# Optimization experiments

Measured on AMD Instinct MI355X. Metric: run time of the kernel, lower is better.

## Reference

```python
import jax, jax.numpy as jnp
import numpy as np

C = 256      # d_model
H = 8        # nhead
DF = 1024    # dim_feedforward
LE = 2048    # ego tokens
LA = 2048    # other-agent tokens
N_MATCH = 1024


def setup_inputs() -> dict:
    key = jax.random.key(0)
    ks = jax.random.split(key, 16)
    def rn(k, shape, s=0.02):
        return jax.random.normal(k, shape, dtype=jnp.float32) * s
    inp = {}
    inp['x_ego'] = jax.random.normal(ks[0], (LE, C), dtype=jnp.float32)
    inp['x_agent'] = jax.random.normal(ks[1], (LA, C), dtype=jnp.float32)
    # query_fusion MLP(2C -> C -> C -> C), torch Linear weight is (out, in)
    inp['Wf1'] = rn(ks[2], (C, 2 * C)); inp['bf1'] = jnp.zeros((C,), jnp.float32)
    inp['Wf2'] = rn(ks[3], (C, C));     inp['bf2'] = jnp.zeros((C,), jnp.float32)
    inp['Wf3'] = rn(ks[4], (C, C));     inp['bf3'] = jnp.zeros((C,), jnp.float32)
    # nn.MultiheadAttention packed in-proj and out-proj
    inp['Wqkv'] = rn(ks[5], (3 * C, C)); inp['bqkv'] = jnp.zeros((3 * C,), jnp.float32)
    inp['Wo'] = rn(ks[6], (C, C));       inp['bo'] = jnp.zeros((C,), jnp.float32)
    # FFN
    inp['W1'] = rn(ks[7], (DF, C)); inp['b1'] = jnp.zeros((DF,), jnp.float32)
    inp['W2'] = rn(ks[8], (C, DF)); inp['b2'] = jnp.zeros((C,), jnp.float32)
    # LayerNorms
    inp['g1'] = jnp.ones((C,), jnp.float32); inp['be1'] = jnp.zeros((C,), jnp.float32)
    inp['g2'] = jnp.ones((C,), jnp.float32); inp['be2'] = jnp.zeros((C,), jnp.float32)
    # unique 1D positions: first N_MATCH agent positions overlap ego, rest don't
    inp['pos_ego'] = jnp.arange(LE, dtype=jnp.int32)
    pa = np.concatenate([np.arange(N_MATCH), np.arange(LA - N_MATCH) + 10_000_000])
    inp['pos_agent'] = jnp.asarray(pa, dtype=jnp.int32)
    inp['n_remain'] = LA - N_MATCH  # static python int
    return inp


def _ln(t, g, b):
    m = t.mean(-1, keepdims=True)
    v = t.var(-1, keepdims=True)
    return (t - m) / jnp.sqrt(v + 1e-5) * g + b


def reference(x_ego, x_agent, Wf1, bf1, Wf2, bf2, Wf3, bf3, Wqkv, bqkv, Wo, bo,
              W1, b1, W2, b2, g1, be1, g2, be2, pos_ego, pos_agent, n_remain):
    # ---- position-keyed grouping / fuse (replaces the host-side dict loop) ----
    eq = pos_agent[:, None] == pos_ego[None, :]          # [La, Le]
    matched_e = eq.any(axis=0)                           # ego token has same-pos agent token
    agent_for_ego = jnp.argmax(eq, axis=0)               # [Le] matching agent index (valid where matched)
    fused_in = jnp.concatenate([x_ego, x_agent[agent_for_ego]], axis=-1)  # [Le, 2C]
    h = jax.nn.relu(fused_in @ Wf1.T + bf1)
    h = jax.nn.relu(h @ Wf2.T + bf2)
    fused = h @ Wf3.T + bf3                              # query_fusion MLP output [Le, C]
    ego_out = jnp.where(matched_e[:, None], fused, x_ego)
    # agent tokens with no ego match, in original agent order (fixed count n_remain)
    remain_idx = jnp.nonzero(~eq.any(axis=1), size=n_remain)[0]
    q = jnp.concatenate([ego_out, x_agent[remain_idx]], axis=0)[None]  # (1, Lq, C)
    kv = jnp.concatenate([x_ego, x_agent], axis=0)[None]               # (1, Lk, C)
    # ---- MultiheadAttention (batch_first, eval: dropout off) ----
    Wq, Wk, Wv = jnp.split(Wqkv, 3, axis=0)
    bq, bk, bv = jnp.split(bqkv, 3, axis=0)
    dh = C // H
    def heads(t, W, b):
        return (t @ W.T + b).reshape(1, -1, H, dh).transpose(0, 2, 1, 3)
    qh, kh, vh = heads(q, Wq, bq), heads(kv, Wk, bk), heads(kv, Wv, bv)
    scores = jnp.einsum('bhqd,bhkd->bhqk', qh, kh) / (float(dh) ** 0.5)
    attn = jax.nn.softmax(scores, axis=-1)
    o = jnp.einsum('bhqk,bhkd->bhqd', attn, vh).transpose(0, 2, 1, 3).reshape(1, -1, C)
    o = o @ Wo.T + bo
    # ---- residual + norm1 + FFN + residual + norm2 ----
    yq = _ln(q + o, g1, be1)
    ff = jax.nn.relu(yq @ W1.T + b1) @ W2.T + b2
    return _ln(yq + ff, g2, be2)
```

## Files before the change

### kernel.cpp

```cpp
#include <hip/hip_runtime.h>


#define LE 2048
#define LA 2048
#define CDIM 256
#define HN 8
#define DH 32
#define DFF 1024
#define NREM 1024
#define LQC 3072
#define LKC 4096
#define KSPLIT 8
#define NIT (LKC / KSPLIT / 64)

typedef unsigned short u16;
typedef unsigned int u32;
typedef __attribute__((ext_vector_type(8))) short bf16x8;
typedef __attribute__((ext_vector_type(4))) float f32x4;

__device__ __forceinline__ u32 pk_bf16(float a, float b) {
    u32 ua = (__builtin_bit_cast(u32, a) + 0x8000u) >> 16;
    u32 ub = (__builtin_bit_cast(u32, b) + 0x8000u) >> 16;
    return ua | (ub << 16);
}
__device__ __forceinline__ u16 bf16_1(float a) {
    return (u16)((__builtin_bit_cast(u32, a) + 0x8000u) >> 16);
}
__device__ __forceinline__ float fast_exp2(float x) {
    return __builtin_amdgcn_exp2f(x);
}
__device__ __forceinline__ bf16x8 ld_pack8(const float* p) {
    float4 f0 = *(const float4*)p;
    float4 f1 = *(const float4*)(p + 4);
    union { u32 u[4]; bf16x8 v; } o;
    o.u[0] = pk_bf16(f0.x, f0.y); o.u[1] = pk_bf16(f0.z, f0.w);
    o.u[2] = pk_bf16(f1.x, f1.y); o.u[3] = pk_bf16(f1.z, f1.w);
    return o.v;
}

__device__ __forceinline__ void xcd_tile(int& bm, int& bn) {
    int gx = gridDim.x;
    int tot = gx * gridDim.y;
    int p = blockIdx.y * gx + blockIdx.x;
    int l = p;
    if (!(tot & 7)) { int c = p & 7, s = p >> 3; l = c * (tot >> 3) + s; }
    bm = (l / gx) * 64;
    bn = (l % gx) * 64;
}

struct WPtrs { const float* p[7]; };
__constant__ __device__ const int woff[8] = {0, 131072, 196608, 262144,
                                             458752, 524288, 786432, 1048576};

__global__ __launch_bounds__(1024) void k_prep(const int* __restrict__ pos_ego,
                                               const int* __restrict__ pos_agent,
                                               int* __restrict__ afe,
                                               int* __restrict__ matched,
                                               int* __restrict__ remain,
                                               const float* __restrict__ x_ego,
                                               const float* __restrict__ x_agent,
                                               WPtrs wp, u16* __restrict__ wb,
                                               u16* __restrict__ kv_b) {
    const int b = blockIdx.x;
    const int t = threadIdx.x;
    if (b == 0) {
        __shared__ int keyA[4096], valA[4096], keyE[4096];
        __shared__ int unm[2048];
#pragma unroll
        for (int i = 0; i < 4; ++i) { keyA[t + i * 1024] = -1; keyE[t + i * 1024] = -1; }
        __syncthreads();
// ... 63 lines not shown
#pragma unroll
        for (int i = 1; i < 7; ++i) s += (g >= woff[i]);
        const float* src = wp.p[s] + (g - woff[s]);
        float4 f0 = *(const float4*)(src);
        float4 f1 = *(const float4*)(src + 4);
        uint4 o;
        o.x = pk_bf16(f0.x, f0.y); o.y = pk_bf16(f0.z, f0.w);
        o.z = pk_bf16(f1.x, f1.y); o.w = pk_bf16(f1.z, f1.w);
        *(uint4*)(wb + g) = o;
    } else {
        int tt = (b - 129) * 1024 + t;
        int j = tt >> 5, c8 = tt & 31;
        const float* src = (j < LE) ? (x_ego + (size_t)j * CDIM)
                                    : (x_agent + (size_t)(j - LE) * CDIM);
        float4 f0 = *(const float4*)(src + c8 * 8);
        float4 f1 = *(const float4*)(src + c8 * 8 + 4);
        uint4 o;
        o.x = pk_bf16(f0.x, f0.y); o.y = pk_bf16(f0.z, f0.w);
        o.z = pk_bf16(f1.x, f1.y); o.w = pk_bf16(f1.z, f1.w);
        *(uint4*)(kv_b + (size_t)j * CDIM + c8 * 8) = o;
    }
}

template <int EPI, bool RELU>
__global__ __launch_bounds__(256) void gemm_bf16(const u16* __restrict__ A,
                                                 const u16* __restrict__ B,
                                                 const float* __restrict__ bias,
                                                 void* __restrict__ C,
                                                 int M, int N, int K) {
    const int tid = threadIdx.x;
    const int w = tid >> 6, lane = tid & 63;
    const int quad = lane >> 4, qi = lane & 15;
    const int wm = w >> 1, wn = w & 1;
    int bm, bn;
    xcd_tile(bm, bn);

    const u16* pa0 = A + (size_t)(bm + wm * 32 + qi) * K + quad * 8;
    const u16* pa1 = pa0 + (size_t)16 * K;
    const u16* pb0 = B + (size_t)(bn + wn * 32 + qi) * K + quad * 8;
    const u16* pb1 = pb0 + (size_t)16 * K;

    f32x4 acc00 = {0.f, 0.f, 0.f, 0.f}, acc01 = {0.f, 0.f, 0.f, 0.f};
    f32x4 acc10 = {0.f, 0.f, 0.f, 0.f}, acc11 = {0.f, 0.f, 0.f, 0.f};

#pragma unroll 4
    for (int k = 0; k < K; k += 32) {
        bf16x8 a0 = *(const bf16x8*)(pa0 + k);
        bf16x8 a1 = *(const bf16x8*)(pa1 + k);
        bf16x8 b0 = *(const bf16x8*)(pb0 + k);
        bf16x8 b1 = *(const bf16x8*)(pb1 + k);
        acc00 = __builtin_amdgcn_mfma_f32_16x16x32_bf16(a0, b0, acc00, 0, 0, 0);
        acc01 = __builtin_amdgcn_mfma_f32_16x16x32_bf16(a0, b1, acc01, 0, 0, 0);
        acc10 = __builtin_amdgcn_mfma_f32_16x16x32_bf16(a1, b0, acc10, 0, 0, 0);
        acc11 = __builtin_amdgcn_mfma_f32_16x16x32_bf16(a1, b1, acc11, 0, 0, 0);
    }

#pragma unroll
    for (int i = 0; i < 2; ++i) {
#pragma unroll
        for (int j = 0; j < 2; ++j) {
            f32x4 acc = (i == 0) ? (j == 0 ? acc00 : acc01) : (j == 0 ? acc10 : acc11);
            int n = bn + wn * 32 + j * 16 + qi;
            int mbase = bm + wm * 32 + i * 16 + quad * 4;
            float bs = bias[n];
            float v[4];
#pragma unroll
            for (int r = 0; r < 4; ++r) {
                float x = acc[r] + bs;
                if (RELU) x = fmaxf(x, 0.f);
                v[r] = x;
            }
            if (EPI == 0) {
                float* Cf = (float*)C;
#pragma unroll
                for (int r = 0; r < 4; ++r) Cf[(size_t)(mbase + r) * N + n] = v[r];
            } else {
                u16* Cb = (u16*)C;
#pragma unroll
                for (int r = 0; r < 4; ++r) Cb[(size_t)(mbase + r) * N + n] = bf16_1(v[r]);
            }
        }
    }
}

__global__ __launch_bounds__(256) void k_mlp1(const float* __restrict__ x_ego,
                                              const float* __restrict__ x_agent,
                                              const int* __restrict__ afe,
                                              const u16* __restrict__ Wf1_b,
                                              const float* __restrict__ bf1,
                                              u16* __restrict__ h1_b) {
    const int tid = threadIdx.x;
    const int w = tid >> 6, lane = tid & 63;
    const int quad = lane >> 4, qi = lane & 15;
    const int wm = w >> 1, wn = w & 1;
    int bm, bn;
    xcd_tile(bm, bn);

    const int r0 = bm + wm * 32 + qi, r1 = r0 + 16;
    const float* pe0 = x_ego + (size_t)r0 * CDIM + quad * 8;
    const float* pe1 = x_ego + (size_t)r1 * CDIM + quad * 8;
    const float* pg0 = x_agent + (size_t)afe[r0] * CDIM + quad * 8;
    const float* pg1 = x_agent + (size_t)afe[r1] * CDIM + quad * 8;
    const u16* pb0 = Wf1_b + (size_t)(bn + wn * 32 + qi) * 512 + quad * 8;
    const u16* pb1 = pb0 + (size_t)16 * 512;

    f32x4 acc00 = {0.f, 0.f, 0.f, 0.f}, acc01 = {0.f, 0.f, 0.f, 0.f};
    f32x4 acc10 = {0.f, 0.f, 0.f, 0.f}, acc11 = {0.f, 0.f, 0.f, 0.f};

#pragma unroll 4
    for (int k = 0; k < 256; k += 32) {
        bf16x8 a0 = ld_pack8(pe0 + k);
        bf16x8 a1 = ld_pack8(pe1 + k);
        bf16x8 b0 = *(const bf16x8*)(pb0 + k);
        bf16x8 b1 = *(const bf16x8*)(pb1 + k);
        acc00 = __builtin_amdgcn_mfma_f32_16x16x32_bf16(a0, b0, acc00, 0, 0, 0);
        acc01 = __builtin_amdgcn_mfma_f32_16x16x32_bf16(a0, b1, acc01, 0, 0, 0);
        acc10 = __builtin_amdgcn_mfma_f32_16x16x32_bf16(a1, b0, acc10, 0, 0, 0);
        acc11 = __builtin_amdgcn_mfma_f32_16x16x32_bf16(a1, b1, acc11, 0, 0, 0);
    }
#pragma unroll 4
    for (int k = 0; k < 256; k += 32) {
        bf16x8 a0 = ld_pack8(pg0 + k);
        bf16x8 a1 = ld_pack8(pg1 + k);
        bf16x8 b0 = *(const bf16x8*)(pb0 + 256 + k);
        bf16x8 b1 = *(const bf16x8*)(pb1 + 256 + k);
        acc00 = __builtin_amdgcn_mfma_f32_16x16x32_bf16(a0, b0, acc00, 0, 0, 0);
        acc01 = __builtin_amdgcn_mfma_f32_16x16x32_bf16(a0, b1, acc01, 0, 0, 0);
        acc10 = __builtin_amdgcn_mfma_f32_16x16x32_bf16(a1, b0, acc10, 0, 0, 0);
        acc11 = __builtin_amdgcn_mfma_f32_16x16x32_bf16(a1, b1, acc11, 0, 0, 0);
    }
#pragma unroll
    for (int i = 0; i < 2; ++i)
#pragma unroll
        for (int j = 0; j < 2; ++j) {
            f32x4 acc = (i == 0) ? (j == 0 ? acc00 : acc01) : (j == 0 ? acc10 : acc11);
            int n = bn + wn * 32 + j * 16 + qi;
            int mbase = bm + wm * 32 + i * 16 + quad * 4;
            float bs = bf1[n];
#pragma unroll
            for (int r = 0; r < 4; ++r) {
                float x = fmaxf(acc[r] + bs, 0.f);
                h1_b[(size_t)(mbase + r) * 256 + n] = bf16_1(x);
            }
        }
}

__global__ __launch_bounds__(256) void k_mlp3f(const u16* __restrict__ h2_b,
                                               const u16* __restrict__ Wf3_b,
                                               const float* __restrict__ bf3,
                                               const int* __restrict__ matched,
                                               const int* __restrict__ remain,
                                               const float* __restrict__ x_ego,
                                               const float* __restrict__ x_agent,
                                               float* __restrict__ qbuf,
                                               u16* __restrict__ qbuf_b) {
    const int tid = threadIdx.x;
    int bm, bn;
    xcd_tile(bm, bn);
    if (bm >= LE) {
        int row = bm + (tid >> 2);
        int col = bn + (tid & 3) * 16;
        int idx = remain[row - LE];
        idx = min(max(idx, 0), LA - 1);
        const float* src = x_agent + (size_t)idx * CDIM + col;
        float* dq = qbuf + (size_t)row * CDIM + col;
        u16* db = qbuf_b + (size_t)row * CDIM + col;
#pragma unroll
        for (int i = 0; i < 4; ++i) {
            float4 v = *(const float4*)(src + i * 4);
            *(float4*)(dq + i * 4) = v;
            *(uint2*)(db + i * 4) = make_uint2(pk_bf16(v.x, v.y), pk_bf16(v.z, v.w));
        }
        return;
    }
    const int w = tid >> 6, lane = tid & 63;
    const int quad = lane >> 4, qi = lane & 15;
    const int wm = w >> 1, wn = w & 1;
    const u16* pa0 = h2_b + (size_t)(bm + wm * 32 + qi) * 256 + quad * 8;
    const u16* pa1 = pa0 + (size_t)16 * 256;
    const u16* pb0 = Wf3_b + (size_t)(bn + wn * 32 + qi) * 256 + quad * 8;
    const u16* pb1 = pb0 + (size_t)16 * 256;
    f32x4 a00 = {0, 0, 0, 0}, a01 = {0, 0, 0, 0}, a10 = {0, 0, 0, 0}, a11 = {0, 0, 0, 0};
#pragma unroll 4
    for (int k = 0; k < 256; k += 32) {
        bf16x8 x0 = *(const bf16x8*)(pa0 + k);
        bf16x8 x1 = *(const bf16x8*)(pa1 + k);
        bf16x8 y0 = *(const bf16x8*)(pb0 + k);
        bf16x8 y1 = *(const bf16x8*)(pb1 + k);
        a00 = __builtin_amdgcn_mfma_f32_16x16x32_bf16(x0, y0, a00, 0, 0, 0);
        a01 = __builtin_amdgcn_mfma_f32_16x16x32_bf16(x0, y1, a01, 0, 0, 0);
        a10 = __builtin_amdgcn_mfma_f32_16x16x32_bf16(x1, y0, a10, 0, 0, 0);
        a11 = __builtin_amdgcn_mfma_f32_16x16x32_bf16(x1, y1, a11, 0, 0, 0);
    }
#pragma unroll
    for (int i = 0; i < 2; ++i)
#pragma unroll
        for (int jj = 0; jj < 2; ++jj) {
            f32x4 acc = (i == 0) ? (jj == 0 ? a00 : a01) : (jj == 0 ? a10 : a11);
            int n = bn + wn * 32 + jj * 16 + qi;
            int mb = bm + wm * 32 + i * 16 + quad * 4;
            float bs = bf3[n];
#pragma unroll
            for (int r = 0; r < 4; ++r) {
                int row = mb + r;
                float v = acc[r] + bs;
                if (!matched[row]) v = x_ego[(size_t)row * CDIM + n];
                qbuf[(size_t)row * CDIM + n] = v;
                qbuf_b[(size_t)row * CDIM + n] = bf16_1(v);
            }
        }
}

__global__ __launch_bounds__(256) void k_qkv(const u16* __restrict__ qbuf_b,
                                             const u16* __restrict__ kv_b,
                                             const u16* __restrict__ Wq,
                                             const u16* __restrict__ Wkv,
                                             const float* __restrict__ bqkv,
                                             u16* __restrict__ qb,
                                             u16* __restrict__ kbp,
                                             u16* __restrict__ vtb,
                                             float qscale) {
    int b;
    {
        int p = blockIdx.x;
        int c = p & 7, s = p >> 3;
        b = c * 88 + s;
    }
    const u16 *A, *B;
    const float* bias;
    int bm, bn, mode;
    if (b < 192) {
        A = qbuf_b; B = Wq; bias = bqkv;
        bm = (b >> 2) * 64; bn = (b & 3) * 64; mode = 0;
// ... 1 lines not shown
        int c = b - 192;
        A = kv_b; B = Wkv; bias = bqkv + 256;
        bm = (c >> 3) * 64; bn = (c & 7) * 64; mode = 1;
    }
    const int tid = threadIdx.x;
    const int w = tid >> 6, lane = tid & 63;
    const int quad = lane >> 4, qi = lane & 15;
    const int wm = w >> 1, wn = w & 1;
    const int K = 256;

    const u16* pa0 = A + (size_t)(bm + wm * 32 + qi) * K + quad * 8;
    const u16* pa1 = pa0 + (size_t)16 * K;
    const u16* pb0 = B + (size_t)(bn + wn * 32 + qi) * K + quad * 8;
    const u16* pb1 = pb0 + (size_t)16 * K;

    f32x4 acc00 = {0.f, 0.f, 0.f, 0.f}, acc01 = {0.f, 0.f, 0.f, 0.f};
    f32x4 acc10 = {0.f, 0.f, 0.f, 0.f}, acc11 = {0.f, 0.f, 0.f, 0.f};
#pragma unroll 4
    for (int k = 0; k < 256; k += 32) {
        bf16x8 a0 = *(const bf16x8*)(pa0 + k);
        bf16x8 a1 = *(const bf16x8*)(pa1 + k);
        bf16x8 b0 = *(const bf16x8*)(pb0 + k);
        bf16x8 b1 = *(const bf16x8*)(pb1 + k);
        acc00 = __builtin_amdgcn_mfma_f32_16x16x32_bf16(a0, b0, acc00, 0, 0, 0);
        acc01 = __builtin_amdgcn_mfma_f32_16x16x32_bf16(a0, b1, acc01, 0, 0, 0);
        acc10 = __builtin_amdgcn_mfma_f32_16x16x32_bf16(a1, b0, acc10, 0, 0, 0);
        acc11 = __builtin_amdgcn_mfma_f32_16x16x32_bf16(a1, b1, acc11, 0, 0, 0);
    }
#pragma unroll
    for (int i = 0; i < 2; ++i) {
#pragma unroll
        for (int j = 0; j < 2; ++j) {
            f32x4 acc = (i == 0) ? (j == 0 ? acc00 : acc01) : (j == 0 ? acc10 : acc11);
            int n = bn + wn * 32 + j * 16 + qi;
            int mbase = bm + wm * 32 + i * 16 + quad * 4;
            float bs = bias[n];
            float v[4];
#pragma unroll
            for (int r = 0; r < 4; ++r) v[r] = acc[r] + bs;
            if (mode == 0) {
#pragma unroll
                for (int r = 0; r < 4; ++r)
                    qb[(size_t)(mbase + r) * 256 + n] = bf16_1(v[r] * qscale);
            } else if (n < 256) {
#pragma unroll
                for (int r = 0; r < 4; ++r)
                    kbp[(size_t)(mbase + r) * 256 + n] = bf16_1(v[r]);
            } else {
                ushort4 o4;
                o4.x = bf16_1(v[0]); o4.y = bf16_1(v[1]);
// ... 50 lines not shown

    int kt = ks * (LKC / KSPLIT);
    {
        bf16x8 kr = *(const bf16x8*)(kg0 + (size_t)kt * CDIM);
        bf16x8 vr = *(const bf16x8*)(vg0 + kt);
        *(bf16x8*)&Kt[0][kdst] = kr;
        *(bf16x8*)&Vt[0][vdst] = vr;
    }
    int buf = 0;
    for (int it = 0; it < NIT; ++it, kt += 64) {
        __syncthreads();
        bf16x8 knext, vnext;
        const bool more = (it + 1 < NIT);
        if (more) {
            knext = *(const bf16x8*)(kg0 + (size_t)(kt + 64) * CDIM);
            vnext = *(const bf16x8*)(vg0 + kt + 64);
        }

        bf16x8 a0 = *(const bf16x8*)&Kt[buf][ka0];
        bf16x8 a1 = *(const bf16x8*)&Kt[buf][ka0 + 16 * 32];
        bf16x8 a2 = *(const bf16x8*)&Kt[buf][ka0 + 32 * 32];
        bf16x8 a3 = *(const bf16x8*)&Kt[buf][ka0 + 48 * 32];
        f32x4 z = {0.f, 0.f, 0.f, 0.f};
        f32x4 s0 = __builtin_amdgcn_mfma_f32_16x16x32_bf16(a0, qf, z, 0, 0, 0);
        f32x4 s1 = __builtin_amdgcn_mfma_f32_16x16x32_bf16(a1, qf, z, 0, 0, 0);
        f32x4 s2 = __builtin_amdgcn_mfma_f32_16x16x32_bf16(a2, qf, z, 0, 0, 0);
        f32x4 s3 = __builtin_amdgcn_mfma_f32_16x16x32_bf16(a3, qf, z, 0, 0, 0);

        float p0[4], p1[4], p2[4], p3[4];
#pragma unroll
        for (int r = 0; r < 4; ++r) {
            p0[r] = fast_exp2(s0[r]); p1[r] = fast_exp2(s1[r]);
            p2[r] = fast_exp2(s2[r]); p3[r] = fast_exp2(s3[r]);
            lsum += p0[r] + p1[r] + p2[r] + p3[r];
        }

        u16* pb = &plds[w][0];
#pragma unroll
        for (int t2 = 0; t2 < 4; ++t2) {
            int jg = t2 * 2 + (quad >> 1);
            int off = qi * 64 + ((jg ^ swz) << 3) + half;
            uint2 pw;
            float* pp = (t2 == 0) ? p0 : (t2 == 1) ? p1 : (t2 == 2) ? p2 : p3;
            pw.x = pk_bf16(pp[0], pp[1]);
            pw.y = pk_bf16(pp[2], pp[3]);
            *(uint2*)&pb[off] = pw;
        }
        bf16x8 pa0 = *(bf16x8*)&pb[rd0];
        bf16x8 pa1 = *(bf16x8*)&pb[rd1];

        bf16x8 v00 = *(const bf16x8*)&Vt[buf][v00o];
        bf16x8 v01 = *(const bf16x8*)&Vt[buf][v01o];
        bf16x8 v10 = *(const bf16x8*)&Vt[buf][v00o + 16 * 64];
        bf16x8 v11 = *(const bf16x8*)&Vt[buf][v01o + 16 * 64];
        O0 = __builtin_amdgcn_mfma_f32_16x16x32_bf16(pa0, v00, O0, 0, 0, 0);
        O0 = __builtin_amdgcn_mfma_f32_16x16x32_bf16(pa1, v01, O0, 0, 0, 0);
        O1 = __builtin_amdgcn_mfma_f32_16x16x32_bf16(pa0, v10, O1, 0, 0, 0);
        O1 = __builtin_amdgcn_mfma_f32_16x16x32_bf16(pa1, v11, O1, 0, 0, 0);

        if (more) {
            *(bf16x8*)&Kt[buf ^ 1][kdst] = knext;
            *(bf16x8*)&Vt[buf ^ 1][vdst] = vnext;
        }
        buf ^= 1;
    }

    lsum += __shfl_xor(lsum, 16, 64);
    lsum += __shfl_xor(lsum, 32, 64);

    int pbase = (h * KSPLIT + ks) * LQC + q0;
    if (quad == 0) Pl[pbase + qi] = lsum;
#pragma unroll
    for (int r = 0; r < 4; ++r) {
        int q = quad * 4 + r;
        u16* pa = Pacc + (size_t)(pbase + q) * 32;
        pa[qi] = __builtin_bit_cast(u16, (_Float16)O0[r]);
        pa[16 + qi] = __builtin_bit_cast(u16, (_Float16)O1[r]);
    }
}

__global__ __launch_bounds__(256) void attn_combine(const float* __restrict__ Pl,
                                                    const u16* __restrict__ Pacc,
                                                    u16* __restrict__ attn_b) {
    int t = blockIdx.x * 256 + threadIdx.x;
    int row = t >> 6;
    int h = (t >> 3) & 7;
    int d4 = t & 7;
    float L = 0.f;
    float o[4] = {};
#pragma unroll
    for (int ck = 0; ck < KSPLIT; ++ck) {
        size_t pidx = (size_t)(h * KSPLIT + ck) * LQC + row;
        L += Pl[pidx];
        ushort4 a = *(const ushort4*)(Pacc + pidx * 32 + d4 * 4);
        o[0] += (float)__builtin_bit_cast(_Float16, a.x);
        o[1] += (float)__builtin_bit_cast(_Float16, a.y);
        o[2] += (float)__builtin_bit_cast(_Float16, a.z);
        o[3] += (float)__builtin_bit_cast(_Float16, a.w);
    }
    float inv = 1.0f / L;
    ushort4 ov;
    ov.x = bf16_1(o[0] * inv); ov.y = bf16_1(o[1] * inv);
    ov.z = bf16_1(o[2] * inv); ov.w = bf16_1(o[3] * inv);
    *(ushort4*)(attn_b + (size_t)row * CDIM + h * DH + d4 * 4) = ov;
}

template <bool EMIT_BF16>
__global__ __launch_bounds__(256) void ln_kernel(const float* __restrict__ X,
                                                 const float* __restrict__ R,
                                                 const float* __restrict__ g,
                                                 const float* __restrict__ b,
                                                 float* __restrict__ out,
                                                 u16* __restrict__ out_b) {
    int lane = threadIdx.x & 63;
    int row = blockIdx.x * 4 + (threadIdx.x >> 6);
    const float* x = X + (size_t)row * CDIM;
    const float* r = R + (size_t)row * CDIM;
    float4 xv = *(const float4*)(x + lane * 4);
    float4 rv = *(const float4*)(r + lane * 4);
    float v[4] = {xv.x + rv.x, xv.y + rv.y, xv.z + rv.z, xv.w + rv.w};
    float s = v[0] + v[1] + v[2] + v[3];
    float sq = v[0] * v[0] + v[1] * v[1] + v[2] * v[2] + v[3] * v[3];
#pragma unroll
    for (int off = 32; off >= 1; off >>= 1) {
        s += __shfl_xor(s, off, 64);
        sq += __shfl_xor(sq, off, 64);
    }
    float mean = s * (1.f / 256.f);
    float var = sq * (1.f / 256.f) - mean * mean;
    float rstd = rsqrtf(var + 1e-5f);
    float4 gv = *(const float4*)(g + lane * 4);
    float4 bv = *(const float4*)(b + lane * 4);
    float4 o = make_float4((v[0] - mean) * rstd * gv.x + bv.x,
                           (v[1] - mean) * rstd * gv.y + bv.y,
                           (v[2] - mean) * rstd * gv.z + bv.z,
                           (v[3] - mean) * rstd * gv.w + bv.w);
    *(float4*)(out + (size_t)row * CDIM + lane * 4) = o;
    if (EMIT_BF16) {
        uint2 ob;
        ob.x = pk_bf16(o.x, o.y);
        ob.y = pk_bf16(o.z, o.w);
        *(uint2*)(out_b + (size_t)row * CDIM + lane * 4) = ob;
    }
}

extern "C" void kernel_launch(void* const* d_in, const int* in_sizes, int n_in,
                              void* d_out, int out_size, void* d_ws, size_t ws_size,
                              hipStream_t stream) {
    const float* x_ego = (const float*)d_in[0];
    const float* x_agent = (const float*)d_in[1];
    const float* Wf1 = (const float*)d_in[2];
    const float* bf1 = (const float*)d_in[3];
    const float* Wf2 = (const float*)d_in[4];
    const float* bf2 = (const float*)d_in[5];
    const float* Wf3 = (const float*)d_in[6];
    const float* bf3 = (const float*)d_in[7];
    const float* Wqkv = (const float*)d_in[8];
    const float* bqkv = (const float*)d_in[9];
    const float* Wo = (const float*)d_in[10];
    const float* bo = (const float*)d_in[11];
    const float* W1 = (const float*)d_in[12];
    const float* b1 = (const float*)d_in[13];
    const float* W2 = (const float*)d_in[14];
    const float* b2 = (const float*)d_in[15];
    const float* g1 = (const float*)d_in[16];
    const float* be1 = (const float*)d_in[17];
    const float* g2 = (const float*)d_in[18];
    const float* be2 = (const float*)d_in[19];
    const int* pos_ego = (const int*)d_in[20];
    const int* pos_agent = (const int*)d_in[21];

    float* ws = (float*)d_ws;
    size_t o = 0;
    float* qbuf = ws + o; o += 786432;
    float* o2 = ws + o; o += 786432;
    float* yq = ws + o; o += 786432;
    float* ff2 = o2;
    float* Pl = ws + o; o += HN * KSPLIT * LQC;
    u16* Pacc = (u16*)(ws + o); o += (size_t)HN * KSPLIT * LQC * 16;
    u16* wb = (u16*)(ws + o); o += 524288;
    u16* h1_b = (u16*)(ws + o); o += 262144;
    u16* h2_b = (u16*)(ws + o); o += 262144;
    u16* qbuf_b = (u16*)(ws + o); o += 393216;
    u16* kv_b = (u16*)(ws + o); o += 524288;
    u16* qb = (u16*)(ws + o); o += 393216;
    u16* kb = (u16*)(ws + o); o += 524288;
    u16* vtb = (u16*)(ws + o); o += 524288;
    u16* attn_b = (u16*)(ws + o); o += 393216;
    u16* ff1_b = (u16*)(ws + o); o += 1572864;
    u16* yq_b = (u16*)(ws + o); o += 393216;
    int* afe = (int*)(ws + o);
    int* matched = afe + LE;
    int* remain = matched + LE;

    const u16* Wf1_b = wb + 0;
    const u16* Wf2_b = wb + 131072;
    const u16* Wf3_b = wb + 196608;
    const u16* Wq_b = wb + 262144;
    const u16* Wkv_b = wb + 327680;
    const u16* Wo_b = wb + 458752;
    const u16* W1_b = wb + 524288;
    const u16* W2_b = wb + 786432;

    WPtrs wp;
    wp.p[0] = Wf1; wp.p[1] = Wf2; wp.p[2] = Wf3; wp.p[3] = Wqkv;
    wp.p[4] = Wo; wp.p[5] = W1; wp.p[6] = W2;

    k_prep<<<257, 1024, 0, stream>>>(pos_ego, pos_agent, afe, matched, remain,
                                     x_ego, x_agent, wp, wb, kv_b);

    const float qscale = 0.17677669529663687f * 1.4426950408889634f;

    k_mlp1<<<dim3(4, 32), 256, 0, stream>>>(x_ego, x_agent, afe, Wf1_b, bf1, h1_b);
    gemm_bf16<1, true><<<dim3(4, 32), 256, 0, stream>>>(h1_b, Wf2_b, bf2, h2_b,
                                                        LE, 256, 256);
    k_mlp3f<<<dim3(4, 48), 256, 0, stream>>>(h2_b, Wf3_b, bf3, matched, remain,
                                             x_ego, x_agent, qbuf, qbuf_b);

    k_qkv<<<704, 256, 0, stream>>>(qbuf_b, kv_b, Wq_b, Wkv_b, bqkv, qb, kb, vtb, qscale);

    attn_mfma<<<dim3(LQC / 64, HN, KSPLIT), 256, 0, stream>>>(qb, kb, vtb, Pl, Pacc);
    attn_combine<<<(LQC * 64) / 256, 256, 0, stream>>>(Pl, Pacc, attn_b);

    gemm_bf16<0, false><<<dim3(4, 48), 256, 0, stream>>>(attn_b, Wo_b, bo, o2,
                                                         LQC, 256, 256);
    ln_kernel<true><<<LQC / 4, 256, 0, stream>>>(qbuf, o2, g1, be1, yq, yq_b);

    gemm_bf16<1, true><<<dim3(16, 48), 256, 0, stream>>>(yq_b, W1_b, b1, ff1_b,
                                                         LQC, DFF, 256);
    gemm_bf16<0, false><<<dim3(4, 48), 256, 0, stream>>>(ff1_b, W2_b, b2, ff2,
                                                         LQC, 256, DFF);
    ln_kernel<false><<<LQC / 4, 256, 0, stream>>>(yq, ff2, g2, be2, (float*)d_out, nullptr);
}
```

Measured before the change: 221.4 us.

## Fuse MLP chain, attention combine+out-proj+LN, and FFN+LN into row-block kernels

Replaces the three query-fusion GEMM launches with one kernel that keeps the intermediate activations for a 16-row block in swizzled shared memory. It also merges attention split-K combine, output projection, residual and LayerNorm into one kernel, and FFN up/down projections with the residual and second LayerNorm into another. This removes several launches and global round trips of intermediates such as h1, h2, attn_b, o2, ff1 and ff2. In exchange the grids are smaller (128-192 blocks of 16 rows), and weight reuse across blocks depends on cache, so parallelism and occupancy may be lower.

```diff
diff --git a/kernel.cpp b/kernel.cpp
--- a/kernel.cpp
+++ b/kernel.cpp
@@ -16,7 +16,10 @@
 typedef unsigned short u16;
 typedef unsigned int u32;
 typedef __attribute__((ext_vector_type(8))) short bf16x8;
+typedef __attribute__((ext_vector_type(8))) _Float16 f16x8;
 typedef __attribute__((ext_vector_type(4))) float f32x4;
+
+#define MFMA __builtin_amdgcn_mfma_f32_16x16x32_bf16
 
 __device__ __forceinline__ u32 pk_bf16(float a, float b) {
     u32 ua = (__builtin_bit_cast(u32, a) + 0x8000u) >> 16;
@@ -36,16 +39,6 @@
     o.u[0] = pk_bf16(f0.x, f0.y); o.u[1] = pk_bf16(f0.z, f0.w);
     o.u[2] = pk_bf16(f1.x, f1.y); o.u[3] = pk_bf16(f1.z, f1.w);
     return o.v;
-}
-
-__device__ __forceinline__ void xcd_tile(int& bm, int& bn) {
-    int gx = gridDim.x;
-    int tot = gx * gridDim.y;
-    int p = blockIdx.y * gx + blockIdx.x;
-    int l = p;
-    if (!(tot & 7)) { int c = p & 7, s = p >> 3; l = c * (tot >> 3) + s; }
-    bm = (l / gx) * 64;
-    bn = (l % gx) * 64;
 }
 
 struct WPtrs { const float* p[7]; };
@@ -155,193 +148,137 @@
     }
 }
 
-template <int EPI, bool RELU>
-__global__ __launch_bounds__(256) void gemm_bf16(const u16* __restrict__ A,
-                                                 const u16* __restrict__ B,
-                                                 const float* __restrict__ bias,
-                                                 void* __restrict__ C,
-                                                 int M, int N, int K) {
-    const int tid = threadIdx.x;
-    const int w = tid >> 6, lane = tid & 63;
-    const int quad = lane >> 4, qi = lane & 15;
-    const int wm = w >> 1, wn = w & 1;
-    int bm, bn;
-    xcd_tile(bm, bn);
-
-    const u16* pa0 = A + (size_t)(bm + wm * 32 + qi) * K + quad * 8;
-    const u16* pa1 = pa0 + (size_t)16 * K;
-    const u16* pb0 = B + (size_t)(bn + wn * 32 + qi) * K + quad * 8;
-    const u16* pb1 = pb0 + (size_t)16 * K;
-
-    f32x4 acc00 = {0.f, 0.f, 0.f, 0.f}, acc01 = {0.f, 0.f, 0.f, 0.f};
-    f32x4 acc10 = {0.f, 0.f, 0.f, 0.f}, acc11 = {0.f, 0.f, 0.f, 0.f};
-
-#pragma unroll 4
-    for (int k = 0; k < K; k += 32) {
-        bf16x8 a0 = *(const bf16x8*)(pa0 + k);
-        bf16x8 a1 = *(const bf16x8*)(pa1 + k);
-        bf16x8 b0 = *(const bf16x8*)(pb0 + k);
-        bf16x8 b1 = *(const bf16x8*)(pb1 + k);
-        acc00 = __builtin_amdgcn_mfma_f32_16x16x32_bf16(a0, b0, acc00, 0, 0, 0);
-        acc01 = __builtin_amdgcn_mfma_f32_16x16x32_bf16(a0, b1, acc01, 0, 0, 0);
-        acc10 = __builtin_amdgcn_mfma_f32_16x16x32_bf16(a1, b0, acc10, 0, 0, 0);
-        acc11 = __builtin_amdgcn_mfma_f32_16x16x32_bf16(a1, b1, acc11, 0, 0, 0);
-    }
-
-#pragma unroll
-    for (int i = 0; i < 2; ++i) {
-#pragma unroll
-        for (int j = 0; j < 2; ++j) {
-            f32x4 acc = (i == 0) ? (j == 0 ? acc00 : acc01) : (j == 0 ? acc10 : acc11);
-            int n = bn + wn * 32 + j * 16 + qi;
-            int mbase = bm + wm * 32 + i * 16 + quad * 4;
-            float bs = bias[n];
-            float v[4];
-#pragma unroll
-            for (int r = 0; r < 4; ++r) {
-                float x = acc[r] + bs;
-                if (RELU) x = fmaxf(x, 0.f);
-                v[r] = x;
-            }
-            if (EPI == 0) {
-                float* Cf = (float*)C;
-#pragma unroll
-                for (int r = 0; r < 4; ++r) Cf[(size_t)(mbase + r) * N + n] = v[r];
-            } else {
-                u16* Cb = (u16*)C;
-#pragma unroll
-                for (int r = 0; r < 4; ++r) Cb[(size_t)(mbase + r) * N + n] = bf16_1(v[r]);
-            }
-        }
-    }
-}
-
-__global__ __launch_bounds__(256) void k_mlp1(const float* __restrict__ x_ego,
+__global__ __launch_bounds__(256) void k_fmlp(const float* __restrict__ x_ego,
                                               const float* __restrict__ x_agent,
                                               const int* __restrict__ afe,
+                                              const int* __restrict__ matched,
+                                              const int* __restrict__ remain,
                                               const u16* __restrict__ Wf1_b,
+                                              const u16* __restrict__ Wf2_b,
+                                              const u16* __restrict__ Wf3_b,
                                               const float* __restrict__ bf1,
-                                              u16* __restrict__ h1_b) {
+                                              const float* __restrict__ bf2,
+                                              const float* __restrict__ bf3,
+                                              float* __restrict__ qbuf,
+                                              u16* __restrict__ qbuf_b) {
+    const int blk = blockIdx.x;
     const int tid = threadIdx.x;
-    const int w = tid >> 6, lane = tid & 63;
-    const int quad = lane >> 4, qi = lane & 15;
-    const int wm = w >> 1, wn = w & 1;
-    int bm, bn;
-    xcd_tile(bm, bn);
-
-    const int r0 = bm + wm * 32 + qi, r1 = r0 + 16;
-    const float* pe0 = x_ego + (size_t)r0 * CDIM + quad * 8;
-    const float* pe1 = x_ego + (size_t)r1 * CDIM + quad * 8;
-    const float* pg0 = x_agent + (size_t)afe[r0] * CDIM + quad * 8;
-    const float* pg1 = x_agent + (size_t)afe[r1] * CDIM + quad * 8;
-    const u16* pb0 = Wf1_b + (size_t)(bn + wn * 32 + qi) * 512 + quad * 8;
-    const u16* pb1 = pb0 + (size_t)16 * 512;
-
-    f32x4 acc00 = {0.f, 0.f, 0.f, 0.f}, acc01 = {0.f, 0.f, 0.f, 0.f};
-    f32x4 acc10 = {0.f, 0.f, 0.f, 0.f}, acc11 = {0.f, 0.f, 0.f, 0.f};
-
-#pragma unroll 4
-    for (int k = 0; k < 256; k += 32) {
-        bf16x8 a0 = ld_pack8(pe0 + k);
-        bf16x8 a1 = ld_pack8(pe1 + k);
-        bf16x8 b0 = *(const bf16x8*)(pb0 + k);
-        bf16x8 b1 = *(const bf16x8*)(pb1 + k);
-        acc00 = __builtin_amdgcn_mfma_f32_16x16x32_bf16(a0, b0, acc00, 0, 0, 0);
-        acc01 = __builtin_amdgcn_mfma_f32_16x16x32_bf16(a0, b1, acc01, 0, 0, 0);
-        acc10 = __builtin_amdgcn_mfma_f32_16x16x32_bf16(a1, b0, acc10, 0, 0, 0);
-        acc11 = __builtin_amdgcn_mfma_f32_16x16x32_bf16(a1, b1, acc11, 0, 0, 0);
-    }
-#pragma unroll 4
-    for (int k = 0; k < 256; k += 32) {
-        bf16x8 a0 = ld_pack8(pg0 + k);
-        bf16x8 a1 = ld_pack8(pg1 + k);
-        bf16x8 b0 = *(const bf16x8*)(pb0 + 256 + k);
-        bf16x8 b1 = *(const bf16x8*)(pb1 + 256 + k);
-        acc00 = __builtin_amdgcn_mfma_f32_16x16x32_bf16(a0, b0, acc00, 0, 0, 0);
-        acc01 = __builtin_amdgcn_mfma_f32_16x16x32_bf16(a0, b1, acc01, 0, 0, 0);
-        acc10 = __builtin_amdgcn_mfma_f32_16x16x32_bf16(a1, b0, acc10, 0, 0, 0);
-        acc11 = __builtin_amdgcn_mfma_f32_16x16x32_bf16(a1, b1, acc11, 0, 0, 0);
-    }
-#pragma unroll
-    for (int i = 0; i < 2; ++i)
-#pragma unroll
-        for (int j = 0; j < 2; ++j) {
-            f32x4 acc = (i == 0) ? (j == 0 ? acc00 : acc01) : (j == 0 ? acc10 : acc11);
-            int n = bn + wn * 32 + j * 16 + qi;
-            int mbase = bm + wm * 32 + i * 16 + quad * 4;
-            float bs = bf1[n];
-#pragma unroll
-            for (int r = 0; r < 4; ++r) {
-                float x = fmaxf(acc[r] + bs, 0.f);
-                h1_b[(size_t)(mbase + r) * 256 + n] = bf16_1(x);
-            }
-        }
-}
-
-__global__ __launch_bounds__(256) void k_mlp3f(const u16* __restrict__ h2_b,
-                                               const u16* __restrict__ Wf3_b,
-                                               const float* __restrict__ bf3,
-                                               const int* __restrict__ matched,
-                                               const int* __restrict__ remain,
-                                               const float* __restrict__ x_ego,
-                                               const float* __restrict__ x_agent,
-                                               float* __restrict__ qbuf,
-                                               u16* __restrict__ qbuf_b) {
-    const int tid = threadIdx.x;
-    int bm, bn;
-    xcd_tile(bm, bn);
-    if (bm >= LE) {
-        int row = bm + (tid >> 2);
-        int col = bn + (tid & 3) * 16;
-        int idx = remain[row - LE];
+    if (blk >= 128) {
+        int rb = (blk - 128) * 64 + (tid >> 2);
+        int row = LE + rb;
+        int col = (tid & 3) * 64;
+        int idx = remain[rb];
         idx = min(max(idx, 0), LA - 1);
         const float* src = x_agent + (size_t)idx * CDIM + col;
         float* dq = qbuf + (size_t)row * CDIM + col;
         u16* db = qbuf_b + (size_t)row * CDIM + col;
 #pragma unroll
-        for (int i = 0; i < 4; ++i) {
+        for (int i = 0; i < 16; ++i) {
             float4 v = *(const float4*)(src + i * 4);
             *(float4*)(dq + i * 4) = v;
             *(uint2*)(db + i * 4) = make_uint2(pk_bf16(v.x, v.y), pk_bf16(v.z, v.w));
         }
         return;
     }
-    const int w = tid >> 6, lane = tid & 63;
-    const int quad = lane >> 4, qi = lane & 15;
-    const int wm = w >> 1, wn = w & 1;
-    const u16* pa0 = h2_b + (size_t)(bm + wm * 32 + qi) * 256 + quad * 8;
-    const u16* pa1 = pa0 + (size_t)16 * 256;
-    const u16* pb0 = Wf3_b + (size_t)(bn + wn * 32 + qi) * 256 + quad * 8;
-    const u16* pb1 = pb0 + (size_t)16 * 256;
-    f32x4 a00 = {0, 0, 0, 0}, a01 = {0, 0, 0, 0}, a10 = {0, 0, 0, 0}, a11 = {0, 0, 0, 0};
-#pragma unroll 4
-    for (int k = 0; k < 256; k += 32) {
-        bf16x8 x0 = *(const bf16x8*)(pa0 + k);
-        bf16x8 x1 = *(const bf16x8*)(pa1 + k);
-        bf16x8 y0 = *(const bf16x8*)(pb0 + k);
-        bf16x8 y1 = *(const bf16x8*)(pb1 + k);
-        a00 = __builtin_amdgcn_mfma_f32_16x16x32_bf16(x0, y0, a00, 0, 0, 0);
-        a01 = __builtin_amdgcn_mfma_f32_16x16x32_bf16(x0, y1, a01, 0, 0, 0);
-        a10 = __builtin_amdgcn_mfma_f32_16x16x32_bf16(x1, y0, a10, 0, 0, 0);
-        a11 = __builtin_amdgcn_mfma_f32_16x16x32_bf16(x1, y1, a11, 0, 0, 0);
-    }
-#pragma unroll
-    for (int i = 0; i < 2; ++i)
-#pragma unroll
-        for (int jj = 0; jj < 2; ++jj) {
-            f32x4 acc = (i == 0) ? (jj == 0 ? a00 : a01) : (jj == 0 ? a10 : a11);
-            int n = bn + wn * 32 + jj * 16 + qi;
-            int mb = bm + wm * 32 + i * 16 + quad * 4;
-            float bs = bf3[n];
+    __shared__ u16 h1[16 * 256];
+    __shared__ u16 h2[16 * 256];
+    const int w = tid >> 6, lane = tid & 63, quad = lane >> 4, qi = lane & 15;
+    const int R0 = blk * 16;
+    const int rg = R0 + qi;
+    {
+        const float* pe = x_ego + (size_t)rg * CDIM + quad * 8;
+        const float* pg = x_agent + (size_t)afe[rg] * CDIM + quad * 8;
+        f32x4 acc[4] = {};
+        const u16* pb = Wf1_b + (size_t)(w * 64 + qi) * 512 + quad * 8;
+#pragma unroll
+        for (int kk = 0; kk < 256; kk += 32) {
+            bf16x8 a = ld_pack8(pe + kk);
+#pragma unroll
+            for (int j = 0; j < 4; ++j) {
+                bf16x8 bfr = *(const bf16x8*)(pb + (size_t)j * 16 * 512 + kk);
+                acc[j] = MFMA(a, bfr, acc[j], 0, 0, 0);
+            }
+        }
+#pragma unroll
+        for (int kk = 0; kk < 256; kk += 32) {
+            bf16x8 a = ld_pack8(pg + kk);
+#pragma unroll
+            for (int j = 0; j < 4; ++j) {
+                bf16x8 bfr = *(const bf16x8*)(pb + (size_t)j * 16 * 512 + 256 + kk);
+                acc[j] = MFMA(a, bfr, acc[j], 0, 0, 0);
+            }
+        }
+#pragma unroll
+        for (int j = 0; j < 4; ++j) {
+            int col = w * 64 + j * 16 + qi;
+            float bs = bf1[col];
 #pragma unroll
             for (int r = 0; r < 4; ++r) {
-                int row = mb + r;
-                float v = acc[r] + bs;
-                if (!matched[row]) v = x_ego[(size_t)row * CDIM + n];
-                qbuf[(size_t)row * CDIM + n] = v;
-                qbuf_b[(size_t)row * CDIM + n] = bf16_1(v);
-            }
-        }
+                int row = quad * 4 + r;
+                float v = fmaxf(acc[j][r] + bs, 0.f);
+                int byte = (row * 512 + col * 2) ^ ((row & 7) << 4);
+                *(u16*)((char*)h1 + byte) = bf16_1(v);
+            }
+        }
+    }
+    __syncthreads();
+    {
+        f32x4 acc[4] = {};
+        const u16* pb = Wf2_b + (size_t)(w * 64 + qi) * 256 + quad * 8;
+#pragma unroll
+        for (int kk = 0; kk < 256; kk += 32) {
+            int byte = (qi * 512 + (kk + quad * 8) * 2) ^ ((qi & 7) << 4);
+            bf16x8 a = *(const bf16x8*)((char*)h1 + byte);
+#pragma unroll
+            for (int j = 0; j < 4; ++j) {
+                bf16x8 bfr = *(const bf16x8*)(pb + (size_t)j * 16 * 256 + kk);
+                acc[j] = MFMA(a, bfr, acc[j], 0, 0, 0);
+            }
+        }
+#pragma unroll
+        for (int j = 0; j < 4; ++j) {
+            int col = w * 64 + j * 16 + qi;
+            float bs = bf2[col];
+#pragma unroll
+            for (int r = 0; r < 4; ++r) {
+                int row = quad * 4 + r;
+                float v = fmaxf(acc[j][r] + bs, 0.f);
+                int byte = (row * 512 + col * 2) ^ ((row & 7) << 4);
+                *(u16*)((char*)h2 + byte) = bf16_1(v);
+            }
+        }
+    }
+    __syncthreads();
+    {
+        f32x4 acc[4] = {};
+        const u16* pb = Wf3_b + (size_t)(w * 64 + qi) * 256 + quad * 8;
+#pragma unroll
+        for (int kk = 0; kk < 256; kk += 32) {
+            int byte = (qi * 512 + (kk + quad * 8) * 2) ^ ((qi & 7) << 4);
+            bf16x8 a = *(const bf16x8*)((char*)h2 + byte);
+#pragma unroll
+            for (int j = 0; j < 4; ++j) {
+                bf16x8 bfr = *(const bf16x8*)(pb + (size_t)j * 16 * 256 + kk);
+                acc[j] = MFMA(a, bfr, acc[j], 0, 0, 0);
+            }
+        }
+        int m[4];
+#pragma unroll
+        for (int r = 0; r < 4; ++r) m[r] = matched[R0 + quad * 4 + r];
+#pragma unroll
+        for (int j = 0; j < 4; ++j) {
+            int col = w * 64 + j * 16 + qi;
+            float bs = bf3[col];
+#pragma unroll
+            for (int r = 0; r < 4; ++r) {
+                int row = R0 + quad * 4 + r;
+                float v = acc[j][r] + bs;
+                if (!m[r]) v = x_ego[(size_t)row * CDIM + col];
+                qbuf[(size_t)row * CDIM + col] = v;
+                qbuf_b[(size_t)row * CDIM + col] = bf16_1(v);
+            }
+        }
+    }
 }
 
 __global__ __launch_bounds__(256) void k_qkv(const u16* __restrict__ qbuf_b,
@@ -389,10 +326,10 @@
         bf16x8 a1 = *(const bf16x8*)(pa1 + k);
         bf16x8 b0 = *(const bf16x8*)(pb0 + k);
         bf16x8 b1 = *(const bf16x8*)(pb1 + k);
-        acc00 = __builtin_amdgcn_mfma_f32_16x16x32_bf16(a0, b0, acc00, 0, 0, 0);
-        acc01 = __builtin_amdgcn_mfma_f32_16x16x32_bf16(a0, b1, acc01, 0, 0, 0);
-        acc10 = __builtin_amdgcn_mfma_f32_16x16x32_bf16(a1, b0, acc10, 0, 0, 0);
-        acc11 = __builtin_amdgcn_mfma_f32_16x16x32_bf16(a1, b1, acc11, 0, 0, 0);
+        acc00 = MFMA(a0, b0, acc00, 0, 0, 0);
+        acc01 = MFMA(a0, b1, acc01, 0, 0, 0);
+        acc10 = MFMA(a1, b0, acc10, 0, 0, 0);
+        acc11 = MFMA(a1, b1, acc11, 0, 0, 0);
     }
 #pragma unroll
     for (int i = 0; i < 2; ++i) {
@@ -489,10 +426,10 @@
         bf16x8 a2 = *(const bf16x8*)&Kt[buf][ka0 + 32 * 32];
         bf16x8 a3 = *(const bf16x8*)&Kt[buf][ka0 + 48 * 32];
         f32x4 z = {0.f, 0.f, 0.f, 0.f};
-        f32x4 s0 = __builtin_amdgcn_mfma_f32_16x16x32_bf16(a0, qf, z, 0, 0, 0);
-        f32x4 s1 = __builtin_amdgcn_mfma_f32_16x16x32_bf16(a1, qf, z, 0, 0, 0);
-        f32x4 s2 = __builtin_amdgcn_mfma_f32_16x16x32_bf16(a2, qf, z, 0, 0, 0);
-        f32x4 s3 = __builtin_amdgcn_mfma_f32_16x16x32_bf16(a3, qf, z, 0, 0, 0);
+        f32x4 s0 = MFMA(a0, qf, z, 0, 0, 0);
+        f32x4 s1 = MFMA(a1, qf, z, 0, 0, 0);
+        f32x4 s2 = MFMA(a2, qf, z, 0, 0, 0);
+        f32x4 s3 = MFMA(a3, qf, z, 0, 0, 0);
 
         float p0[4], p1[4], p2[4], p3[4];
 #pragma unroll
@@ -520,10 +457,10 @@
         bf16x8 v01 = *(const bf16x8*)&Vt[buf][v01o];
         bf16x8 v10 = *(const bf16x8*)&Vt[buf][v00o + 16 * 64];
         bf16x8 v11 = *(const bf16x8*)&Vt[buf][v01o + 16 * 64];
-        O0 = __builtin_amdgcn_mfma_f32_16x16x32_bf16(pa0, v00, O0, 0, 0, 0);
-        O0 = __builtin_amdgcn_mfma_f32_16x16x32_bf16(pa1, v01, O0, 0, 0, 0);
-        O1 = __builtin_amdgcn_mfma_f32_16x16x32_bf16(pa0, v10, O1, 0, 0, 0);
-        O1 = __builtin_amdgcn_mfma_f32_16x16x32_bf16(pa1, v11, O1, 0, 0, 0);
+        O0 = MFMA(pa0, v00, O0, 0, 0, 0);
+        O0 = MFMA(pa1, v01, O0, 0, 0, 0);
+        O1 = MFMA(pa0, v10, O1, 0, 0, 0);
+        O1 = MFMA(pa1, v11, O1, 0, 0, 0);
 
         if (more) {
             *(bf16x8*)&Kt[buf ^ 1][kdst] = knext;
@@ -546,68 +483,214 @@
     }
 }
 
-__global__ __launch_bounds__(256) void attn_combine(const float* __restrict__ Pl,
-                                                    const u16* __restrict__ Pacc,
-                                                    u16* __restrict__ attn_b) {
-    int t = blockIdx.x * 256 + threadIdx.x;
-    int row = t >> 6;
-    int h = (t >> 3) & 7;
-    int d4 = t & 7;
-    float L = 0.f;
-    float o[4] = {};
-#pragma unroll
-    for (int ck = 0; ck < KSPLIT; ++ck) {
-        size_t pidx = (size_t)(h * KSPLIT + ck) * LQC + row;
-        L += Pl[pidx];
-        ushort4 a = *(const ushort4*)(Pacc + pidx * 32 + d4 * 4);
-        o[0] += (float)__builtin_bit_cast(_Float16, a.x);
-        o[1] += (float)__builtin_bit_cast(_Float16, a.y);
-        o[2] += (float)__builtin_bit_cast(_Float16, a.z);
-        o[3] += (float)__builtin_bit_cast(_Float16, a.w);
-    }
-    float inv = 1.0f / L;
-    ushort4 ov;
-    ov.x = bf16_1(o[0] * inv); ov.y = bf16_1(o[1] * inv);
-    ov.z = bf16_1(o[2] * inv); ov.w = bf16_1(o[3] * inv);
-    *(ushort4*)(attn_b + (size_t)row * CDIM + h * DH + d4 * 4) = ov;
-}
-
-template <bool EMIT_BF16>
-__global__ __launch_bounds__(256) void ln_kernel(const float* __restrict__ X,
-                                                 const float* __restrict__ R,
-                                                 const float* __restrict__ g,
-                                                 const float* __restrict__ b,
-                                                 float* __restrict__ out,
-                                                 u16* __restrict__ out_b) {
-    int lane = threadIdx.x & 63;
-    int row = blockIdx.x * 4 + (threadIdx.x >> 6);
-    const float* x = X + (size_t)row * CDIM;
-    const float* r = R + (size_t)row * CDIM;
-    float4 xv = *(const float4*)(x + lane * 4);
-    float4 rv = *(const float4*)(r + lane * 4);
-    float v[4] = {xv.x + rv.x, xv.y + rv.y, xv.z + rv.z, xv.w + rv.w};
-    float s = v[0] + v[1] + v[2] + v[3];
-    float sq = v[0] * v[0] + v[1] * v[1] + v[2] * v[2] + v[3] * v[3];
-#pragma unroll
-    for (int off = 32; off >= 1; off >>= 1) {
-        s += __shfl_xor(s, off, 64);
-        sq += __shfl_xor(sq, off, 64);
-    }
-    float mean = s * (1.f / 256.f);
-    float var = sq * (1.f / 256.f) - mean * mean;
-    float rstd = rsqrtf(var + 1e-5f);
-    float4 gv = *(const float4*)(g + lane * 4);
-    float4 bv = *(const float4*)(b + lane * 4);
-    float4 o = make_float4((v[0] - mean) * rstd * gv.x + bv.x,
-                           (v[1] - mean) * rstd * gv.y + bv.y,
-                           (v[2] - mean) * rstd * gv.z + bv.z,
-                           (v[3] - mean) * rstd * gv.w + bv.w);
-    *(float4*)(out + (size_t)row * CDIM + lane * 4) = o;
-    if (EMIT_BF16) {
-        uint2 ob;
-        ob.x = pk_bf16(o.x, o.y);
-        ob.y = pk_bf16(o.z, o.w);
-        *(uint2*)(out_b + (size_t)row * CDIM + lane * 4) = ob;
+__global__ __launch_bounds__(256) void k_oln(const float* __restrict__ Pl,
+                                             const u16* __restrict__ Pacc,
+                                             const u16* __restrict__ Wo_b,
+                                             const float* __restrict__ bo,
+                                             const float* __restrict__ qbuf,
+                                             const float* __restrict__ g1,
+                                             const float* __restrict__ be1,
+                                             float* __restrict__ yq,
+                                             u16* __restrict__ yq_b) {
+    __shared__ u16 At[16 * 256];
+    __shared__ float red[16][4][2];
+    const int tid = threadIdx.x;
+    const int R0 = blockIdx.x * 16;
+    {
+        int row = tid >> 4, cg = tid & 15;
+        int h = cg >> 1, dh = (cg & 1) * 16;
+        int r = R0 + row;
+        float L = 0.f;
+        float o[16] = {};
+#pragma unroll
+        for (int ks = 0; ks < 8; ++ks) {
+            size_t pidx = (size_t)(h * 8 + ks) * LQC + r;
+            L += Pl[pidx];
+            const u16* pa = Pacc + pidx * 32 + dh;
+            f16x8 v0 = *(const f16x8*)(pa);
+            f16x8 v1 = *(const f16x8*)(pa + 8);
+#pragma unroll
+            for (int i = 0; i < 8; ++i) {
+                o[i] += (float)v0[i];
+                o[8 + i] += (float)v1[i];
+            }
+        }
+        float invL = 1.0f / L;
+        int cb = h * 32 + dh;
+#pragma unroll
+        for (int i = 0; i < 8; ++i) {
+            int c0 = cb + 2 * i;
+            u32 pk = pk_bf16(o[2 * i] * invL, o[2 * i + 1] * invL);
+            int byte = (row * 512 + c0 * 2) ^ ((row & 7) << 4);
+            *(u32*)((char*)At + byte) = pk;
+        }
+    }
+    __syncthreads();
+    const int w = tid >> 6, lane = tid & 63, quad = lane >> 4, qi = lane & 15;
+    f32x4 acc[4] = {};
+    const u16* pb = Wo_b + (size_t)(w * 64 + qi) * 256 + quad * 8;
+#pragma unroll
+    for (int kk = 0; kk < 256; kk += 32) {
+        int byte = (qi * 512 + (kk + quad * 8) * 2) ^ ((qi & 7) << 4);
+        bf16x8 a = *(const bf16x8*)((char*)At + byte);
+#pragma unroll
+        for (int j = 0; j < 4; ++j) {
+            bf16x8 bfr = *(const bf16x8*)(pb + (size_t)j * 16 * 256 + kk);
+            acc[j] = MFMA(a, bfr, acc[j], 0, 0, 0);
+        }
+    }
+    float v[4][4], s[4] = {}, sq[4] = {};
+#pragma unroll
+    for (int j = 0; j < 4; ++j) {
+        int col = w * 64 + j * 16 + qi;
+        float bs = bo[col];
+#pragma unroll
+        for (int r = 0; r < 4; ++r) {
+            int row = R0 + quad * 4 + r;
+            float x = acc[j][r] + bs + qbuf[(size_t)row * CDIM + col];
+            v[j][r] = x; s[r] += x; sq[r] += x * x;
+        }
+    }
+#pragma unroll
+    for (int off = 1; off < 16; off <<= 1) {
+#pragma unroll
+        for (int r = 0; r < 4; ++r) {
+            s[r] += __shfl_xor(s[r], off, 64);
+            sq[r] += __shfl_xor(sq[r], off, 64);
+        }
+    }
+    if (qi == 0) {
+#pragma unroll
+        for (int r = 0; r < 4; ++r) {
+            red[quad * 4 + r][w][0] = s[r];
+            red[quad * 4 + r][w][1] = sq[r];
+        }
+    }
+    __syncthreads();
+    float mean[4], rstd[4];
+#pragma unroll
+    for (int r = 0; r < 4; ++r) {
+        int rl = quad * 4 + r;
+        float st = red[rl][0][0] + red[rl][1][0] + red[rl][2][0] + red[rl][3][0];
+        float sqt = red[rl][0][1] + red[rl][1][1] + red[rl][2][1] + red[rl][3][1];
+        mean[r] = st * (1.f / 256.f);
+        float var = sqt * (1.f / 256.f) - mean[r] * mean[r];
+        rstd[r] = rsqrtf(var + 1e-5f);
+    }
+#pragma unroll
+    for (int j = 0; j < 4; ++j) {
+        int col = w * 64 + j * 16 + qi;
+        float gg = g1[col], bb = be1[col];
+#pragma unroll
+        for (int r = 0; r < 4; ++r) {
+            int row = R0 + quad * 4 + r;
+            float o = (v[j][r] - mean[r]) * rstd[r] * gg + bb;
+            yq[(size_t)row * CDIM + col] = o;
+            yq_b[(size_t)row * CDIM + col] = bf16_1(o);
+        }
+    }
+}
+
+__global__ __launch_bounds__(256) void k_ffn(const u16* __restrict__ yq_b,
+                                             const float* __restrict__ yq,
+                                             const u16* __restrict__ W1_b,
+                                             const float* __restrict__ b1,
+                                             const u16* __restrict__ W2_b,
+                                             const float* __restrict__ b2,
+                                             const float* __restrict__ g2,
+                                             const float* __restrict__ be2,
+                                             float* __restrict__ out) {
+    __shared__ u16 hT[16 * 1024];
+    __shared__ float red[16][4][2];
+    const int tid = threadIdx.x;
+    const int w = tid >> 6, lane = tid & 63, quad = lane >> 4, qi = lane & 15;
+    const int R0 = blockIdx.x * 16;
+    {
+        const u16* pa = yq_b + (size_t)(R0 + qi) * 256 + quad * 8;
+        f32x4 acc[16] = {};
+        const u16* pb = W1_b + (size_t)(w * 256 + qi) * 256 + quad * 8;
+#pragma unroll
+        for (int kk = 0; kk < 256; kk += 32) {
+            bf16x8 a = *(const bf16x8*)(pa + kk);
+#pragma unroll
+            for (int j = 0; j < 16; ++j) {
+                bf16x8 bfr = *(const bf16x8*)(pb + (size_t)j * 16 * 256 + kk);
+                acc[j] = MFMA(a, bfr, acc[j], 0, 0, 0);
+            }
+        }
+#pragma unroll
+        for (int j = 0; j < 16; ++j) {
+            int col = w * 256 + j * 16 + qi;
+            float bs = b1[col];
+#pragma unroll
+            for (int r = 0; r < 4; ++r) {
+                int row = quad * 4 + r;
+                float v = fmaxf(acc[j][r] + bs, 0.f);
+                int byte = (row * 2048 + col * 2) ^ ((row & 7) << 4);
+                *(u16*)((char*)hT + byte) = bf16_1(v);
+            }
+        }
+    }
+    __syncthreads();
+    f32x4 acc[4] = {};
+    const u16* pb = W2_b + (size_t)(w * 64 + qi) * 1024 + quad * 8;
+#pragma unroll 4
+    for (int kk = 0; kk < 1024; kk += 32) {
+        int byte = (qi * 2048 + (kk + quad * 8) * 2) ^ ((qi & 7) << 4);
+        bf16x8 a = *(const bf16x8*)((char*)hT + byte);
+#pragma unroll
+        for (int j = 0; j < 4; ++j) {
+            bf16x8 bfr = *(const bf16x8*)(pb + (size_t)j * 16 * 1024 + kk);
+            acc[j] = MFMA(a, bfr, acc[j], 0, 0, 0);
+        }
+    }
+    float v[4][4], s[4] = {}, sq[4] = {};
+#pragma unroll
+    for (int j = 0; j < 4; ++j) {
+        int col = w * 64 + j * 16 + qi;
+        float bs = b2[col];
+#pragma unroll
+        for (int r = 0; r < 4; ++r) {
+            int row = R0 + quad * 4 + r;
+            float x = acc[j][r] + bs + yq[(size_t)row * CDIM + col];
+            v[j][r] = x; s[r] += x; sq[r] += x * x;
+        }
+    }
+#pragma unroll
+    for (int off = 1; off < 16; off <<= 1) {
+#pragma unroll
+        for (int r = 0; r < 4; ++r) {
+            s[r] += __shfl_xor(s[r], off, 64);
+            sq[r] += __shfl_xor(sq[r], off, 64);
+        }
+    }
+    if (qi == 0) {
+#pragma unroll
+        for (int r = 0; r < 4; ++r) {
+            red[quad * 4 + r][w][0] = s[r];
+            red[quad * 4 + r][w][1] = sq[r];
+        }
+    }
+    __syncthreads();
+    float mean[4], rstd[4];
+#pragma unroll
+    for (int r = 0; r < 4; ++r) {
+        int rl = quad * 4 + r;
+        float st = red[rl][0][0] + red[rl][1][0] + red[rl][2][0] + red[rl][3][0];
+        float sqt = red[rl][0][1] + red[rl][1][1] + red[rl][2][1] + red[rl][3][1];
+        mean[r] = st * (1.f / 256.f);
+        float var = sqt * (1.f / 256.f) - mean[r] * mean[r];
+        rstd[r] = rsqrtf(var + 1e-5f);
+    }
+#pragma unroll
+    for (int j = 0; j < 4; ++j) {
+        int col = w * 64 + j * 16 + qi;
+        float gg = g2[col], bb = be2[col];
+#pragma unroll
+        for (int r = 0; r < 4; ++r) {
+            int row = R0 + quad * 4 + r;
+            out[(size_t)row * CDIM + col] = (v[j][r] - mean[r]) * rstd[r] * gg + bb;
+        }
     }
 }
 
@@ -640,21 +723,15 @@
     float* ws = (float*)d_ws;
     size_t o = 0;
     float* qbuf = ws + o; o += 786432;
-    float* o2 = ws + o; o += 786432;
     float* yq = ws + o; o += 786432;
-    float* ff2 = o2;
     float* Pl = ws + o; o += HN * KSPLIT * LQC;
     u16* Pacc = (u16*)(ws + o); o += (size_t)HN * KSPLIT * LQC * 16;
     u16* wb = (u16*)(ws + o); o += 524288;
-    u16* h1_b = (u16*)(ws + o); o += 262144;
-    u16* h2_b = (u16*)(ws + o); o += 262144;
     u16* qbuf_b = (u16*)(ws + o); o += 393216;
     u16* kv_b = (u16*)(ws + o); o += 524288;
     u16* qb = (u16*)(ws + o); o += 393216;
     u16* kb = (u16*)(ws + o); o += 524288;
     u16* vtb = (u16*)(ws + o); o += 524288;
-    u16* attn_b = (u16*)(ws + o); o += 393216;
-    u16* ff1_b = (u16*)(ws + o); o += 1572864;
     u16* yq_b = (u16*)(ws + o); o += 393216;
     int* afe = (int*)(ws + o);
     int* matched = afe + LE;
@@ -678,24 +755,16 @@
 
     const float qscale = 0.17677669529663687f * 1.4426950408889634f;
 
-    k_mlp1<<<dim3(4, 32), 256, 0, stream>>>(x_ego, x_agent, afe, Wf1_b, bf1, h1_b);
-    gemm_bf16<1, true><<<dim3(4, 32), 256, 0, stream>>>(h1_b, Wf2_b, bf2, h2_b,
-                                                        LE, 256, 256);
-    k_mlp3f<<<dim3(4, 48), 256, 0, stream>>>(h2_b, Wf3_b, bf3, matched, remain,
-                                             x_ego, x_agent, qbuf, qbuf_b);
+    k_fmlp<<<144, 256, 0, stream>>>(x_ego, x_agent, afe, matched, remain,
+                                    Wf1_b, Wf2_b, Wf3_b, bf1, bf2, bf3,
+                                    qbuf, qbuf_b);
 
     k_qkv<<<704, 256, 0, stream>>>(qbuf_b, kv_b, Wq_b, Wkv_b, bqkv, qb, kb, vtb, qscale);
 
     attn_mfma<<<dim3(LQC / 64, HN, KSPLIT), 256, 0, stream>>>(qb, kb, vtb, Pl, Pacc);
-    attn_combine<<<(LQC * 64) / 256, 256, 0, stream>>>(Pl, Pacc, attn_b);
-
-    gemm_bf16<0, false><<<dim3(4, 48), 256, 0, stream>>>(attn_b, Wo_b, bo, o2,
-                                                         LQC, 256, 256);
-    ln_kernel<true><<<LQC / 4, 256, 0, stream>>>(qbuf, o2, g1, be1, yq, yq_b);
-
-    gemm_bf16<1, true><<<dim3(16, 48), 256, 0, stream>>>(yq_b, W1_b, b1, ff1_b,
-                                                         LQC, DFF, 256);
-    gemm_bf16<0, false><<<dim3(4, 48), 256, 0, stream>>>(ff1_b, W2_b, b2, ff2,
-                                                         LQC, 256, DFF);
-    ln_kernel<false><<<LQC / 4, 256, 0, stream>>>(yq, ff2, g2, be2, (float*)d_out, nullptr);
-}
+
+    k_oln<<<LQC / 16, 256, 0, stream>>>(Pl, Pacc, Wo_b, bo, qbuf, g1, be1, yq, yq_b);
+
+    k_ffn<<<LQC / 16, 256, 0, stream>>>(yq_b, yq, W1_b, b1, W2_b, b2, g2, be2,
+                                        (float*)d_out);
+}
```

Result: no change. 223.0 us (+0.7%).
